# Performance work log

Measured on AMD Instinct MI355X. Metric: run time of the kernel, lower is better.

Reference implementation:

```python
import jax, jax.numpy as jnp
import numpy as np

B, T, N, M, P, YD = 256, 64, 128, 256, 256, 1


def lstm_cell(x, h, c, Wih, Whh, bih, bhh):
    # torch LSTM gate order: i, f, g, o
    gates = x @ Wih.T + h @ Whh.T + bih + bhh  # (B, 4H)
    i, f, g, o = jnp.split(gates, 4, axis=-1)
    c_new = jax.nn.sigmoid(f) * c + jax.nn.sigmoid(i) * jnp.tanh(g)
    h_new = jax.nn.sigmoid(o) * jnp.tanh(c_new)
    return h_new, c_new


def setup_inputs() -> dict:
    key = jax.random.key(0)
    ks = jax.random.split(key, 20)
    s = 0.05
    return {
        "inputs": jax.random.normal(ks[0], (B, T, N + YD), jnp.float32),
        "WU_e": jax.random.normal(ks[1], (T, 2 * M + T), jnp.float32) * s,
        "v_e": jax.random.normal(ks[2], (1, T), jnp.float32) * s,
        "Wih_e": jax.random.normal(ks[3], (4 * M, N), jnp.float32) * s,
        "Whh_e": jax.random.normal(ks[4], (4 * M, M), jnp.float32) * s,
        "bih_e": jax.random.normal(ks[5], (4 * M,), jnp.float32) * s,
        "bhh_e": jax.random.normal(ks[6], (4 * M,), jnp.float32) * s,
        "WU_d": jax.random.normal(ks[7], (M, 2 * P + M), jnp.float32) * s,
        "v_d": jax.random.normal(ks[8], (1, M), jnp.float32) * s,
        "wb_tilde": jax.random.normal(ks[9], (1, YD + M), jnp.float32) * s,
        "Wih_d": jax.random.normal(ks[10], (4 * P, 1), jnp.float32) * s,
        "Whh_d": jax.random.normal(ks[11], (4 * P, P), jnp.float32) * s,
        "bih_d": jax.random.normal(ks[12], (4 * P,), jnp.float32) * s,
        "bhh_d": jax.random.normal(ks[13], (4 * P,), jnp.float32) * s,
        "Wb_W": jax.random.normal(ks[14], (P, P + M), jnp.float32) * s,
        "Wb_b": jax.random.normal(ks[15], (P,), jnp.float32) * s,
        "vb_W": jax.random.normal(ks[16], (YD, P), jnp.float32) * s,
        "vb_b": jax.random.normal(ks[17], (YD,), jnp.float32) * s,
    }


def _darnn(inputs, WU_e, v_e, Wih_e, Whh_e, bih_e, bhh_e,
           WU_d, v_d, wb_tilde, Wih_d, Whh_d, bih_d, bhh_d,
           Wb_W, Wb_b, vb_W, vb_b):
    X = inputs[:, :, :N]          # (B, T, N)
    Y = inputs[:, :, N:]          # (B, T, YD)
    X_nt = jnp.transpose(X, (0, 2, 1))  # (B, N, T), constant across encoder steps

    # ---------------- Encoder ----------------
    def enc_step(carry, x_t):  # x_t: (B, N)
        h, c = carry
        hs = jnp.concatenate([h, c], axis=-1)  # (B, 2M)
        feat = jnp.concatenate(
            [jnp.broadcast_to(hs[:, None, :], (B, N, 2 * M)), X_nt], axis=-1)  # (B, N, 2M+T)
        E = (jnp.tanh(feat @ WU_e.T) @ v_e.T)[..., 0]  # (B, N)
        alpha = jax.nn.softmax(E, axis=1)
        h, c = lstm_cell(x_t * alpha, h, c, Wih_e, Whh_e, bih_e, bhh_e)
        return (h, c), h

    h0 = jnp.zeros((B, M), inputs.dtype)
    c0 = jnp.zeros((B, M), inputs.dtype)
    _, X_encoded = jax.lax.scan(enc_step, (h0, c0), jnp.transpose(X, (1, 0, 2)))
    Xe_bm = jnp.transpose(X_encoded, (1, 0, 2))  # (B, T, M)

    # ---------------- Decoder ----------------
    def dec_step(carry, y_t):  # y_t: (B, YD)
        h, c, _ = carry
        hs = jnp.concatenate([h, c], axis=-1)  # (B, 2P)
        feat = jnp.concatenate(
            [jnp.broadcast_to(hs[:, None, :], (B, T, 2 * P)), Xe_bm], axis=-1)  # (B, T, 2P+M)
        l = (jnp.tanh(feat @ WU_d.T) @ v_d.T)[..., 0]  # (B, T)
        beta = jax.nn.softmax(l, axis=1)
        ctx = jnp.einsum('bt,btm->bm', beta, Xe_bm)  # (B, M)
        y_tilde = jnp.concatenate([y_t, ctx], axis=-1) @ wb_tilde.T  # (B, 1)
        h, c = lstm_cell(y_tilde, h, c, Wih_d, Whh_d, bih_d, bhh_d)
        return (h, c, ctx), None

    hd0 = jnp.zeros((B, P), inputs.dtype)
    cd0 = jnp.zeros((B, P), inputs.dtype)
    ctx0 = jnp.zeros((B, M), inputs.dtype)
    (h, c, ctx), _ = jax.lax.scan(
        dec_step, (hd0, cd0, ctx0), jnp.transpose(Y[:, :T - 1, :], (1, 0, 2)))

    hidden = jnp.concatenate([h, ctx], axis=-1) @ Wb_W.T + Wb_b  # (B, P)
    y_hat = hidden @ vb_W.T + vb_b  # (B, YD)
    return y_hat


def reference(inputs, WU_e, v_e, Wih_e, Whh_e, bih_e, bhh_e,
              WU_d, v_d, wb_tilde, Wih_d, Whh_d, bih_d, bhh_d,
              Wb_W, Wb_b, vb_W, vb_b):
    return _darnn(inputs, WU_e, v_e, Wih_e, Whh_e, bih_e, bhh_e,
                  WU_d, v_d, wb_tilde, Wih_d, Whh_d, bih_d, bhh_d,
                  Wb_W, Wb_b, vb_W, vb_b)
```

## Files before the change

### kernel.cpp

```cpp
#include <hip/hip_runtime.h>
#include <math.h>


#define OFF_XWT   0u
#define OFF_XEWT  2097152u
#define OFF_XE    6291456u
#define OFF_HE    10485760u
#define OFF_HD    10616832u
#define OFF_SB    10747904u
#define OFF_SDB   10780672u
#define OFF_XA    10911744u
#define OFF_CTX   10944512u
#define OFF_YT    11010048u
#define OFF_BAR   11010304u
#define WS_END    11010816u

#define SENT_U 0x7FC00001u

#define SLAB_F 24576
#define PER_F  2432
#define SCR_F  12288
#define FLG_F  16
#define SMEM_F (SLAB_F + PER_F + SCR_F + FLG_F)
#define SMEM_BYTES (SMEM_F * 4)

#define F_E 0
#define F_L 1
#define F_B 2

__device__ __forceinline__ float fast_tanh(float x) {
  float xc = fminf(15.f, fmaxf(-15.f, x));
  float e = __expf(2.f * xc);
  return 1.f - 2.f * __builtin_amdgcn_rcpf(e + 1.f);
}
__device__ __forceinline__ float fast_sig(float x) {
  float xc = fminf(30.f, fmaxf(-30.f, x));
  return __builtin_amdgcn_rcpf(1.f + __expf(-xc));
}
__device__ __forceinline__ float wave_max(float v) {
#pragma unroll
  for (int o = 32; o; o >>= 1) v = fmaxf(v, __shfl_xor(v, o));
  return v;
}
__device__ __forceinline__ float wave_sum(float v) {
#pragma unroll
  for (int o = 32; o; o >>= 1) v += __shfl_xor(v, o);
  return v;
}
__device__ __forceinline__ float dot4(float4 a, float4 b) {
  return a.x*b.x + a.y*b.y + a.z*b.z + a.w*b.w;
}

__device__ __forceinline__ void st1_sc1(float* p, float v) {
  asm volatile("global_store_dword %0, %1, off sc1" :: "v"(p), "v"(v) : "memory");
}
__device__ __forceinline__ void ld1q_sc1(float4& a, const float* pa) {
  asm volatile("global_load_dwordx4 %0, %1, off sc1\n\ts_waitcnt vmcnt(0)"
               : "=&v"(a) : "v"(pa) : "memory");
}
__device__ __forceinline__ void ld1q_nw(float4& a, const float* pa) {
  asm volatile("global_load_dwordx4 %0, %1, off sc1"
               : "=&v"(a) : "v"(pa) : "memory");
}
__device__ __forceinline__ void vm0() {
  asm volatile("s_waitcnt vmcnt(0)" ::: "memory");
}
__device__ __forceinline__ void lgk0() {
  asm volatile("s_waitcnt lgkmcnt(0)" ::: "memory");
}
__device__ __forceinline__ float ld1s_sc1(const float* p) {
  float v;
  asm volatile("global_load_dword %0, %1, off sc1\n\ts_waitcnt vmcnt(0)"
               : "=&v"(v) : "v"(p) : "memory");
  return v;
}
__device__ __forceinline__ void ld8s_sc1(
    float& a0,float& a1,float& a2,float& a3,float& a4,float& a5,float& a6,float& a7,
    const float* p0,const float* p1,const float* p2,const float* p3,
    const float* p4,const float* p5,const float* p6,const float* p7) {
  asm volatile(
      "global_load_dword %0, %8, off sc1\n\t"
      "global_load_dword %1, %9, off sc1\n\t"
      "global_load_dword %2, %10, off sc1\n\t"
      "global_load_dword %3, %11, off sc1\n\t"
      "global_load_dword %4, %12, off sc1\n\t"
      "global_load_dword %5, %13, off sc1\n\t"
      "global_load_dword %6, %14, off sc1\n\t"
      "global_load_dword %7, %15, off sc1\n\t"
      "s_waitcnt vmcnt(0)"
      : "=&v"(a0),"=&v"(a1),"=&v"(a2),"=&v"(a3),
        "=&v"(a4),"=&v"(a5),"=&v"(a6),"=&v"(a7)
      : "v"(p0),"v"(p1),"v"(p2),"v"(p3),"v"(p4),"v"(p5),"v"(p6),"v"(p7)
      : "memory");
}
__device__ __forceinline__ void atomic_add_sc1(float* p, float v) {
  asm volatile("global_atomic_add_f32 %0, %1, off sc1" :: "v"(p), "v"(v) : "memory");
}

__device__ __forceinline__ void lds_inc(unsigned* f) {
  __hip_atomic_fetch_add(f, 1u, __ATOMIC_RELAXED, __HIP_MEMORY_SCOPE_WORKGROUP);
}
__device__ __forceinline__ void lds_poll(unsigned* f, unsigned tgt) {
  unsigned cur;
  do { cur = __hip_atomic_load(f, __ATOMIC_RELAXED, __HIP_MEMORY_SCOPE_WORKGROUP); } while (cur < tgt);
  asm volatile("" ::: "memory");
}

#define FMA16V(a0,a1,a2,a3,xv,wv) \
  a0.x += xv.x*wv.x; a0.y += xv.x*wv.y; a0.z += xv.x*wv.z; a0.w += xv.x*wv.w; \
  a1.x += xv.y*wv.x; a1.y += xv.y*wv.y; a1.z += xv.y*wv.z; a1.w += xv.y*wv.w; \
  a2.x += xv.z*wv.x; a2.y += xv.z*wv.y; a2.z += xv.z*wv.z; a2.w += xv.z*wv.w; \
  a3.x += xv.w*wv.x; a3.y += xv.w*wv.y; a3.z += xv.w*wv.z; a3.w += xv.w*wv.w;

__device__ __forceinline__ void bar_arrive(unsigned* bar) {
  asm volatile("s_waitcnt vmcnt(0)" ::: "memory");
  __syncthreads();
  if (threadIdx.x == 0)
    __hip_atomic_fetch_add(bar, 1u, __ATOMIC_RELAXED, __HIP_MEMORY_SCOPE_AGENT);
}
__device__ __forceinline__ void bar_wait(unsigned* bar, unsigned target) {
  if (threadIdx.x == 0) {
    unsigned cur;
    do {
      __builtin_amdgcn_s_sleep(1);
      cur = __hip_atomic_load(bar, __ATOMIC_RELAXED, __HIP_MEMORY_SCOPE_AGENT);
    } while (cur < target);
  }
  __syncthreads();
}

__global__ void darnn_init(float* __restrict__ ws, float* __restrict__ out) {
  unsigned i = blockIdx.x * 256u + threadIdx.x;
  const unsigned span = WS_END - OFF_HE;
  for (unsigned idx = i; idx < span; idx += gridDim.x * 256u) ws[OFF_HE + idx] = 0.f;
  if (i < 256u) out[i] = 0.f;
}

__global__ __launch_bounds__(512, 2) void darnn_main(
    const float* __restrict__ in,   const float* __restrict__ WUe,   const float* __restrict__ ve,
    const float* __restrict__ Wih_e,const float* __restrict__ Whh_e,
    const float* __restrict__ bih_e,const float* __restrict__ bhh_e,
    const float* __restrict__ WUd,  const float* __restrict__ vd,
    const float* __restrict__ wbt,  const float* __restrict__ Wih_d,
    const float* __restrict__ Whh_d,const float* __restrict__ bih_d, const float* __restrict__ bhh_d,
    const float* __restrict__ WbW,  const float* __restrict__ Wbb,
    const float* __restrict__ vbW,  const float* __restrict__ vbb,
    float* __restrict__ ws, float* __restrict__ out)
{
  extern __shared__ __align__(16) float sm[];
  float* SLAB = sm;
  float* PER  = sm + SLAB_F;
  float* SCR  = sm + SLAB_F + PER_F;
  unsigned* FLG = (unsigned*)(sm + SLAB_F + PER_F + SCR_F);
  const int tid = threadIdx.x;
  const int bid = blockIdx.x;
  const int grp = bid >> 4;
  const int mt  = bid & 15;
  const int b0  = grp << 4;
  const float SENTF = __uint_as_float(SENT_U);

  float* XWt  = ws + OFF_XWT;
  float* XeWt = ws + OFF_XEWT;
  float* Xe   = ws + OFF_XE;
  unsigned* barp = (unsigned*)(ws + OFF_BAR) + grp * 32;
  unsigned barn = 0;

  if (tid < FLG_F) FLG[tid] = 0u;

  float* wue_s  = PER;
  float* ve_s   = PER + 2304;
  float* bsum_e = PER + 2368;

  const int jfixE = ((tid & 63) + mt * 4) & 63;

  {
    int r = tid & 63, kq = tid >> 6;
    int grow = (r & 3) * 256 + mt * 16 + (r >> 2);
#pragma unroll 4
    for (int q = 0; q < 12; ++q) {
      int k = kq * 48 + q * 4;
      float4 wv = (k < 128) ? *(const float4*)(Wih_e + grow * 128 + k)
                            : *(const float4*)(Whh_e + grow * 256 + (k - 128));
      SLAB[(k + 0) * 64 + r] = wv.x; SLAB[(k + 1) * 64 + r] = wv.y;
      SLAB[(k + 2) * 64 + r] = wv.z; SLAB[(k + 3) * 64 + r] = wv.w;
    }
    {
      int lin = tid * 4;
      int j = lin >> 5, c0 = lin & 31;
      int col = (c0 < 16) ? (mt * 16 + c0) : (256 + mt * 16 + (c0 - 16));
      float4 wv = *(const float4*)(WUe + j * 576 + col);
      *(float4*)(wue_s + j * 36 + c0) = wv;
    }
    if (tid < 64) {
      ve_s[tid] = ve[tid];
      int g = tid >> 4, m2 = tid & 15, m = mt * 16 + m2;
      bsum_e[tid] = bih_e[g * 256 + m] + bhh_e[g * 256 + m];
    }
  }

  {
    float* Xs = SCR;
    const float* Xb = in + bid * 8256;
    __syncthreads();
    for (int it = 0; it < 16; ++it) {
      int lin = tid + it * 512;
      int k = lin >> 7, n = lin & 127;
      Xs[n * 68 + k] = Xb[k * 129 + n];
    }
    __syncthreads();
    int j = tid & 63, nh = tid >> 6;
    float acc[16];
#pragma unroll
    for (int i = 0; i < 16; ++i) acc[i] = 0.f;
    const float* wrow = WUe + j * 576 + 512;
    for (int kc = 0; kc < 4; ++kc) {
      float4 w0 = *(const float4*)(wrow + kc * 16 + 0);
      float4 w1 = *(const float4*)(wrow + kc * 16 + 4);
      float4 w2 = *(const float4*)(wrow + kc * 16 + 8);
      float4 w3 = *(const float4*)(wrow + kc * 16 + 12);
#pragma unroll
      for (int ni = 0; ni < 16; ++ni) {
        const float* xp = Xs + (nh * 16 + ni) * 68 + kc * 16;
        acc[ni] += dot4(*(const float4*)(xp + 0),  w0) + dot4(*(const float4*)(xp + 4),  w1)
                 + dot4(*(const float4*)(xp + 8),  w2) + dot4(*(const float4*)(xp + 12), w3);
      }
    }
    float* dst = XWt + bid * 8192 + j * 128 + nh * 16;
#pragma unroll
    for (int ni = 0; ni < 16; ++ni) dst[ni] = acc[ni];
    __syncthreads();
  }

  float4 whc[8];
#pragma unroll
  for (int q = 0; q < 8; ++q) whc[q] = *(const float4*)(wue_s + jfixE * 36 + q * 4);
  float4 bsE = {0,0,0,0};
  {
    int m2 = tid & 15;
    bsE.x = bsum_e[m2]; bsE.y = bsum_e[16 + m2];
    bsE.z = bsum_e[32 + m2]; bsE.w = bsum_e[48 + m2];
  }
  float xwreg[32];
  if (tid < 256) {
    int w = tid >> 6, l = tid & 63;
    const float* xwp = XWt + bid * 8192;
#pragma unroll
    for (int jj = 0; jj < 16; ++jj) {
      xwreg[jj]      = xwp[(w * 16 + jj) * 128 + l];
      xwreg[16 + jj] = xwp[(w * 16 + jj) * 128 + 64 + l];
    }
  }
  float c_reg = 0.f;

  for (int t = 0; t < 64; ++t) {
    const int rd = t & 1, wr2 = (t + 1) & 1;
    float* xah = SCR + 1024;
    const int ks = tid >> 6, ml = (tid >> 2) & 15, b4 = tid & 3;
    float4 a0 = {0,0,0,0}, a1 = {0,0,0,0}, a2 = {0,0,0,0}, a3 = {0,0,0,0};

    bar_wait(barp, barn);

    if (tid < 256) {
      int w = tid >> 6, l = tid & 63;
      float* Sj = SCR;
      float* Ep = SCR + 64;
      if (l < 16)
        Sj[w * 16 + l] = ld1s_sc1(ws + OFF_SB + (unsigned)rd * 16384 + (unsigned)bid * 64 + w * 16 + l);
      lgk0();
      float e0 = 0.f, e1 = 0.f;
#pragma unroll
      for (int jj = 0; jj < 16; ++jj) {
        float s = Sj[w * 16 + jj];
        float vv = ve_s[w * 16 + jj];
        e0 += vv * fast_tanh(xwreg[jj] + s);
        e1 += vv * fast_tanh(xwreg[16 + jj] + s);
      }
      Ep[w * 128 + l] = e0;
      Ep[w * 128 + 64 + l] = e1;
      lgk0();
      if (l == 0) lds_inc(FLG + F_E);
      if (w == 0) {
        lds_poll(FLG + F_E, 4u * (t + 1));
        float En0 = Ep[l] + Ep[128 + l] + Ep[256 + l] + Ep[384 + l];
        float En1 = Ep[64 + l] + Ep[192 + l] + Ep[320 + l] + Ep[448 + l];
        float mx = wave_max(fmaxf(En0, En1));
        float ex0 = __expf(En0 - mx), ex1 = __expf(En1 - mx);
        float tot = wave_sum(ex0 + ex1);
        float rt = __builtin_amdgcn_rcpf(tot);
        float x0 = in[bid * 8256 + t * 129 + l];
        float x1 = in[bid * 8256 + t * 129 + 64 + l];
        float* XAg = ws + OFF_XA + (unsigned)grp * 2048;
        st1_sc1(XAg + l * 16 + mt, x0 * ex0 * rt);
        st1_sc1(XAg + (64 + l) * 16 + mt, x1 * ex1 * rt);
        vm0();
        if (tid == 0)
          __hip_atomic_fetch_add(barp, 1u, __ATOMIC_RELAXED, __HIP_MEMORY_SCOPE_AGENT);
      }
    } else {
      int u = tid - 256;
      float4 h0, h1, h2, h3;
      const float* hb = ws + OFF_HE + (unsigned)rd * 65536 + (unsigned)grp * 4096 + u * 16;
      ld1q_nw(h0, hb); ld1q_nw(h1, hb + 4); ld1q_nw(h2, hb + 8); ld1q_nw(h3, hb + 12);
      vm0();
      float* row = xah + (unsigned)(128 + u) * 20;
      *(float4*)(row + 0) = h0; *(float4*)(row + 4) = h1;
      *(float4*)(row + 8) = h2; *(float4*)(row + 12) = h3;
      lgk0();
      int s = u >> 6;
      const float* xp = xah + (unsigned)(128 + s * 64) * 20 + b4 * 4;
      const float* wp = SLAB + (unsigned)(128 + s * 64) * 64 + ml * 4;
#pragma unroll 8
      for (int kk = 0; kk < 64; ++kk) {
        float4 xv = *(const float4*)(xp + kk * 20);
        float4 wv = *(const float4*)(wp + kk * 64);
        FMA16V(a0, a1, a2, a3, xv, wv);
      }
    }
    barn += 16;
    bar_wait(barp, barn);

    if (tid < 16) {
      float* sp = ws + OFF_SB + (unsigned)rd * 16384 + (unsigned)bid * 64 + tid * 4;
      float z01 = (t == 63 && tid == 0) ? SENTF : 0.f;
      st1_sc1(sp + 0, z01); st1_sc1(sp + 1, z01);
      st1_sc1(sp + 2, 0.f); st1_sc1(sp + 3, 0.f);
    }
    {
      int l = tid & 63;
      int k = (ks << 4) + (l >> 2), i4 = (l & 3) * 4;
      float4 q;
      ld1q_sc1(q, ws + OFF_XA + (unsigned)grp * 2048 + k * 16 + i4);
      *(float4*)(xah + k * 20 + i4) = q;
      lgk0();
    }
    {
      const float* xp = xah + (unsigned)(ks * 16) * 20 + b4 * 4;
      const float* wp = SLAB + (unsigned)(ks * 16) * 64 + ml * 4;
#pragma unroll 8
      for (int kk = 0; kk < 16; ++kk) {
        float4 xv = *(const float4*)(xp + kk * 20);
        float4 wv = *(const float4*)(wp + kk * 64);
        FMA16V(a0, a1, a2, a3, xv, wv);
      }
    }
    __syncthreads();
    float* red = SCR;
    {
      float* rp = red + (unsigned)(ks * 64 + ml * 4 + b4) * 20;
      *(float4*)(rp + 0) = a0; *(float4*)(rp + 4) = a1;
      *(float4*)(rp + 8) = a2; *(float4*)(rp + 12) = a3;
    }
    __syncthreads();
    float* hcs = SCR + 10240;
    if (tid < 256) {
      int m2 = tid & 15, bl = tid >> 4;
      int t2 = m2 * 4 + (bl >> 2), bs = bl & 3;
      float4 gate = {0,0,0,0};
#pragma unroll
      for (int k2 = 0; k2 < 8; ++k2) {
        float4 rr = *(const float4*)(red + (unsigned)(k2 * 64 + t2) * 20 + bs * 4);
        gate.x += rr.x; gate.y += rr.y; gate.z += rr.z; gate.w += rr.w;
      }
      float gi = gate.x + bsE.x, gf = gate.y + bsE.y;
      float gg = gate.z + bsE.z, go = gate.w + bsE.w;
      float cn = fast_sig(gf) * c_reg + fast_sig(gi) * fast_tanh(gg);
      float hn = fast_sig(go) * fast_tanh(cn);
      c_reg = cn;
      unsigned m = mt * 16 + m2;
      st1_sc1(ws + OFF_HE + (unsigned)wr2 * 65536 + (unsigned)grp * 4096 + m * 16 + bl, hn);
      st1_sc1(Xe + ((unsigned)(b0 + bl) * 64 + t) * 256 + m, hn);
      hcs[bl * 32 + m2] = hn;
      hcs[bl * 32 + 16 + m2] = cn;
    }
    __syncthreads();
    {
      int wq = tid >> 6;
#pragma unroll
      for (int e2 = 0; e2 < 2; ++e2) {
        int bl2 = wq * 2 + e2;
        const float* hp = hcs + bl2 * 32;
        float s = 0.f;
#pragma unroll
        for (int q = 0; q < 4; ++q) {
          s += dot4(*(const float4*)(hp + q * 4), whc[q]);
          s += dot4(*(const float4*)(hp + 16 + q * 4), whc[4 + q]);
        }
        atomic_add_sc1(ws + OFF_SB + (unsigned)wr2 * 16384 + (unsigned)(b0 + bl2) * 64 + jfixE, s);
      }
    }
    barn += 16;
    bar_arrive(barp);
  }
  bar_wait(barp, barn);

  float xe[64];
  if (tid < 256) {
    const float* xb = Xe + (unsigned)bid * 16384 + tid;
#pragma unroll
    for (int g8 = 0; g8 < 8; ++g8) {
      ld8s_sc1(xe[g8*8+0], xe[g8*8+1], xe[g8*8+2], xe[g8*8+3],
               xe[g8*8+4], xe[g8*8+5], xe[g8*8+6], xe[g8*8+7],
               xb + (g8*8+0)*256, xb + (g8*8+1)*256, xb + (g8*8+2)*256,
               xb + (g8*8+3)*256, xb + (g8*8+4)*256, xb + (g8*8+5)*256,
               xb + (g8*8+6)*256, xb + (g8*8+7)*256);
    }
  }

  float* vd_s   = PER;
  float* wbt_s  = PER + 256;
  float* bsum_d = PER + 520;
  float* wihd_s = PER + 584;
  float* q_s    = PER + 704;
  float* qpart  = PER + 768;
  float* wudT   = SLAB + 16384;
  const int jfixD = ((tid & 255) + mt * 16) & 255;
  __syncthreads();
  {
    int r = tid & 63, kq = tid >> 6;
    int grow = (r & 3) * 256 + mt * 16 + (r >> 2);
#pragma unroll 4
    for (int q = 0; q < 8; ++q) {
      int k = kq * 32 + q * 4;
      float4 wv = *(const float4*)(Whh_d + grow * 256 + k);
      SLAB[(k + 0) * 64 + r] = wv.x; SLAB[(k + 1) * 64 + r] = wv.y;
      SLAB[(k + 2) * 64 + r] = wv.z; SLAB[(k + 3) * 64 + r] = wv.w;
    }
    {
      int j = tid & 255, half = tid >> 8;
#pragma unroll
      for (int i = 0; i < 16; ++i) {
        int c = half * 16 + i;
        int col = (c < 16) ? (mt * 16 + c) : (256 + mt * 16 + (c - 16));
        wudT[c * 256 + j] = WUd[(unsigned)j * 768 + col];
      }
    }
    if (tid < 256) vd_s[tid] = vd[tid];
    if (tid < 257) wbt_s[tid] = wbt[tid];
    if (tid < 64) {
      int g = tid >> 4, m2 = tid & 15, m = mt * 16 + m2;
      bsum_d[tid] = bih_d[g * 256 + m] + bhh_d[g * 256 + m];
      wihd_s[tid] = Wih_d[g * 256 + m];
    }
  }
  __syncthreads();

  if (tid < 256) {
    int w = tid >> 6, l = tid & 63;
    float wm = wbt_s[1 + tid];
#pragma unroll
    for (int t4 = 0; t4 < 64; ++t4) {
      float v = wave_sum(wm * xe[t4]);
      if (l == 0) qpart[w * 64 + t4] = v;
    }
  }
  __syncthreads();
  if (tid < 64) q_s[tid] = qpart[tid] + qpart[64 + tid] + qpart[128 + tid] + qpart[192 + tid];
  __syncthreads();

  {
    float* XeT = SCR;
    float* Wdc = SCR + 4096;
    int tt2 = tid & 15, jq = tid >> 4;
    for (int jc = 0; jc < 2; ++jc) {
      float4 c0 = {0,0,0,0}, c1 = {0,0,0,0}, c2 = {0,0,0,0}, c3 = {0,0,0,0};
      for (int kc = 0; kc < 4; ++kc) {
        __syncthreads();
        if (tid < 256 && (tid >> 6) == kc) {
          int kk = tid & 63;
#pragma unroll
          for (int t4 = 0; t4 < 16; ++t4) {
            float4 v = { xe[t4*4+0], xe[t4*4+1], xe[t4*4+2], xe[t4*4+3] };
            *(float4*)(XeT + kk * 64 + t4 * 4) = v;
          }
        }
        {
          int jj = tid >> 2, k16 = (tid & 3) * 16;
          const float* src = WUd + (unsigned)(jc * 128 + jj) * 768 + 512 + kc * 64 + k16;
#pragma unroll
          for (int s4 = 0; s4 < 4; ++s4) {
            float4 wv = *(const float4*)(src + s4 * 4);
            Wdc[(k16 + s4*4 + 0) * 128 + jj] = wv.x;
            Wdc[(k16 + s4*4 + 1) * 128 + jj] = wv.y;
            Wdc[(k16 + s4*4 + 2) * 128 + jj] = wv.z;
            Wdc[(k16 + s4*4 + 3) * 128 + jj] = wv.w;
          }
        }
        __syncthreads();
#pragma unroll 8
        for (int kk = 0; kk < 64; ++kk) {
          float4 xv = *(const float4*)(XeT + kk * 64 + tt2 * 4);
          float4 wv = *(const float4*)(Wdc + kk * 128 + jq * 4);
          FMA16V(c0, c1, c2, c3, wv, xv);
        }
      }
      int jb = jc * 128 + jq * 4;
      *(float4*)(XeWt + ((unsigned)bid * 256 + jb + 0) * 64 + tt2 * 4) = c0;
      *(float4*)(XeWt + ((unsigned)bid * 256 + jb + 1) * 64 + tt2 * 4) = c1;
      *(float4*)(XeWt + ((unsigned)bid * 256 + jb + 2) * 64 + tt2 * 4) = c2;
      *(float4*)(XeWt + ((unsigned)bid * 256 + jb + 3) * 64 + tt2 * 4) = c3;
    }
    __syncthreads();
  }

  float wreg[32];
#pragma unroll
  for (int c = 0; c < 32; ++c) wreg[c] = wudT[c * 256 + jfixD];
  float4 bsD = {0,0,0,0}, wiD = {0,0,0,0};
  {
    int m2 = tid & 15;
    bsD.x = bsum_d[m2]; bsD.y = bsum_d[16 + m2]; bsD.z = bsum_d[32 + m2]; bsD.w = bsum_d[48 + m2];
    wiD.x = wihd_s[m2]; wiD.y = wihd_s[16 + m2]; wiD.z = wihd_s[32 + m2]; wiD.w = wihd_s[48 + m2];
  }
  float xewreg[64];
  if (tid < 256) {
    int w = tid >> 6, l = tid & 63;
    const float* xew = XeWt + (unsigned)bid * 16384 + l;
#pragma unroll
    for (int jj = 0; jj < 64; ++jj) xewreg[jj] = xew[(w * 64 + jj) << 6];
  }
  float q_reg = 0.f, yv = 0.f;
  if (tid < 64) {
    q_reg = q_s[tid];
    if (tid < 63) yv = in[bid * 8256 + tid * 129 + 128];
  }
  const float wbt0 = wbt_s[0];
  float cd_reg = 0.f;

  for (int t = 0; t < 63; ++t) {
    const int rd = t & 1, wr2 = (t + 1) & 1;
    const int ml = (tid >> 2) & 15, b4 = tid & 3;
    float* hT  = SCR + 2048;
    float* red = SCR + 7168;

    bar_wait(barp, barn);

    if (tid < 256) {
      int w = tid >> 6, l = tid & 63;
      float* Sdj  = SCR;
      float* lp   = SCR + 256;
      float* beta = SCR + 512;
      Sdj[w * 64 + l] = ld1s_sc1(ws + OFF_SDB + (unsigned)rd * 65536 + (unsigned)bid * 256 + w * 64 + l);
      lgk0();
      float lpar = 0.f;
#pragma unroll 8
      for (int jj = 0; jj < 64; ++jj)
        lpar += vd_s[w * 64 + jj] * fast_tanh(xewreg[jj] + Sdj[w * 64 + jj]);
      lp[w * 64 + l] = lpar;
      lgk0();
      if (l == 0) lds_inc(FLG + F_L);
      if (w == 0) {
        lds_poll(FLG + F_L, 4u * (t + 1));
        float lv = lp[l] + lp[64 + l] + lp[128 + l] + lp[192 + l];
        float mx = wave_max(lv);
        float ex = __expf(lv - mx);
        float sw = wave_sum(ex);
        float rt = __builtin_amdgcn_rcpf(sw);
        float ytn = wave_sum(ex * q_reg);
        if (l == 0) {
          float yt = wbt0 * __shfl(yv, t) + ytn * rt;
          st1_sc1(ws + OFF_SB + 16384u + (unsigned)bid * 64u + (unsigned)rd, yt);
        }
        if (t == 62) {
          beta[l] = ex * rt;
          lgk0();
          if (l == 0) lds_inc(FLG + F_B);
        }
      }
      if (t == 62) {
        lds_poll(FLG + F_B, 1u);
        lgk0();
        float ctx = 0.f;
#pragma unroll
        for (int tt = 0; tt < 64; ++tt) ctx += beta[tt] * xe[tt];
        st1_sc1(ws + OFF_CTX + (unsigned)bid * 256 + tid, ctx);
      }
    } else {
      if (tid == 256)
        st1_sc1(ws + OFF_SB + 16384u + (unsigned)bid * 64u + (unsigned)wr2, SENTF);
      int u = tid - 256;
      float4 h0, h1, h2, h3;
      const float* hb = ws + OFF_HD + (unsigned)rd * 65536 + (unsigned)grp * 4096 + u * 16;
      ld1q_nw(h0, hb); ld1q_nw(h1, hb + 4); ld1q_nw(h2, hb + 8); ld1q_nw(h3, hb + 12);
      vm0();
      float* row = hT + (unsigned)u * 20;
      *(float4*)(row + 0) = h0; *(float4*)(row + 4) = h1;
      *(float4*)(row + 8) = h2; *(float4*)(row + 12) = h3;
      lgk0();
      int s = u >> 6;
      float4 a0 = {0,0,0,0}, a1 = {0,0,0,0}, a2 = {0,0,0,0}, a3 = {0,0,0,0};
      const float* xp = hT + (unsigned)(s * 64) * 20 + b4 * 4;
      const float* wp = SLAB + (unsigned)(s * 64) * 64 + ml * 4;
#pragma unroll 8
      for (int kk = 0; kk < 64; ++kk) {
        float4 xv = *(const float4*)(xp + kk * 20);
        float4 wv = *(const float4*)(wp + kk * 64);
        FMA16V(a0, a1, a2, a3, xv, wv);
      }
      float* rp = red + (unsigned)(s * 64 + ml * 4 + b4) * 20;
      *(float4*)(rp + 0) = a0; *(float4*)(rp + 4) = a1;
      *(float4*)(rp + 8) = a2; *(float4*)(rp + 12) = a3;
    }
    if (tid < 64) {
      float* sp = ws + OFF_SDB + (unsigned)rd * 65536 + (unsigned)bid * 256 + tid * 4;
      st1_sc1(sp + 0, 0.f); st1_sc1(sp + 1, 0.f);
      st1_sc1(sp + 2, 0.f); st1_sc1(sp + 3, 0.f);
    }
    __syncthreads();

    float* hcs = SCR;
    if (tid < 256) {
      int m2 = tid & 15, bl = tid >> 4;
      int t2 = m2 * 4 + (bl >> 2), bs = bl & 3;
      float4 gate = {0,0,0,0};
#pragma unroll
      for (int k2 = 0; k2 < 4; ++k2) {
        float4 rr = *(const float4*)(red + (unsigned)(k2 * 64 + t2) * 20 + bs * 4);
        gate.x += rr.x; gate.y += rr.y; gate.z += rr.z; gate.w += rr.w;
      }
      const float* pyt = ws + OFF_SB + 16384u + (unsigned)(b0 + bl) * 64u + (unsigned)rd;
      float yt_reg = ld1s_sc1(pyt);
      while (__float_as_uint(yt_reg) == SENT_U) {
        __builtin_amdgcn_s_sleep(4);
        yt_reg = ld1s_sc1(pyt);
      }
      float gi = gate.x + yt_reg * wiD.x + bsD.x;
      float gf = gate.y + yt_reg * wiD.y + bsD.y;
      float gg = gate.z + yt_reg * wiD.z + bsD.z;
      float go = gate.w + yt_reg * wiD.w + bsD.w;
      float cn = fast_sig(gf) * cd_reg + fast_sig(gi) * fast_tanh(gg);
      float hn = fast_sig(go) * fast_tanh(cn);
      cd_reg = cn;
      unsigned m = mt * 16 + m2;
      st1_sc1(ws + OFF_HD + (unsigned)wr2 * 65536 + (unsigned)grp * 4096 + m * 16 + bl, hn);
      hcs[bl * 32 + m2] = hn;
      hcs[bl * 32 + 16 + m2] = cn;
    }
    __syncthreads();
    {
      int half = tid >> 8;
#pragma unroll
      for (int e2 = 0; e2 < 8; ++e2) {
        int bl2 = half * 8 + e2;
        const float* hp = hcs + bl2 * 32;
        float s = 0.f;
#pragma unroll
        for (int c = 0; c < 16; ++c) s += hp[c] * wreg[c];
#pragma unroll
        for (int c = 0; c < 16; ++c) s += hp[16 + c] * wreg[16 + c];
        atomic_add_sc1(ws + OFF_SDB + (unsigned)wr2 * 65536 + (unsigned)(b0 + bl2) * 256 + jfixD, s);
      }
    }
    barn += 16;
    bar_arrive(barp);
  }
  bar_wait(barp, barn);

  {
    float* hsf  = SCR;
    float* hid2 = SCR + 8256;
    {
      int l0 = tid * 2, l1 = tid * 2 + 1;
      int k0 = l0 >> 2, i0 = l0 & 3, k1 = l1 >> 2, i1 = l1 & 3;
      const float* hb = ws + OFF_HD + 65536u + (unsigned)grp * 4096;
      int bl0 = l0 >> 6, c0 = (l0 & 63) * 4, bl1 = l1 >> 6, c1 = (l1 & 63) * 4;
      float4 qa, qb, qc, qd;
      ld1q_nw(qa, hb + k0 * 16 + i0 * 4);
      ld1q_nw(qb, hb + k1 * 16 + i1 * 4);
      ld1q_nw(qc, ws + OFF_CTX + (unsigned)(b0 + bl0) * 256 + c0);
      ld1q_nw(qd, ws + OFF_CTX + (unsigned)(b0 + bl1) * 256 + c1);
      vm0();
      hsf[(i0 * 4 + 0) * 516 + k0] = qa.x; hsf[(i0 * 4 + 1) * 516 + k0] = qa.y;
      hsf[(i0 * 4 + 2) * 516 + k0] = qa.z; hsf[(i0 * 4 + 3) * 516 + k0] = qa.w;
      hsf[(i1 * 4 + 0) * 516 + k1] = qb.x; hsf[(i1 * 4 + 1) * 516 + k1] = qb.y;
      hsf[(i1 * 4 + 2) * 516 + k1] = qb.z; hsf[(i1 * 4 + 3) * 516 + k1] = qb.w;
      *(float4*)(hsf + bl0 * 516 + 256 + c0) = qc;
      *(float4*)(hsf + bl1 * 516 + 256 + c1) = qd;
    }
    __syncthreads();
    int bl = tid & 15, p4 = (tid >> 4) & 15, half = tid >> 8;
    int row = mt * 16 + p4;
    const float* wrow = WbW + (unsigned)row * 512 + half * 256;
    const float* hp = hsf + bl * 516 + half * 256;
    float acc = half ? 0.f : Wbb[row];
#pragma unroll 8
    for (int q = 0; q < 64; ++q)
      acc += dot4(*(const float4*)(hp + q * 4), *(const float4*)(wrow + q * 4));
    hid2[half * 272 + bl * 17 + p4] = acc;
    __syncthreads();
    if (tid < 16) {
      float s = 0.f;
#pragma unroll
      for (int p = 0; p < 16; ++p)
        s += (hid2[tid * 17 + p] + hid2[272 + tid * 17 + p]) * vbW[mt * 16 + p];
      if (mt == 0) s += vbb[0];
      atomicAdd(&out[b0 + tid], s);
    }
  }
}

extern "C" void kernel_launch(void* const* d_in, const int* in_sizes, int n_in,
                              void* d_out, int out_size, void* d_ws, size_t ws_size,
                              hipStream_t stream) {
  (void)in_sizes; (void)n_in; (void)out_size; (void)ws_size;
  const float* in    = (const float*)d_in[0];
  const float* WUe   = (const float*)d_in[1];
  const float* ve    = (const float*)d_in[2];
  const float* Wih_e = (const float*)d_in[3];
  const float* Whh_e = (const float*)d_in[4];
  const float* bih_e = (const float*)d_in[5];
  const float* bhh_e = (const float*)d_in[6];
  const float* WUd   = (const float*)d_in[7];
  const float* vd    = (const float*)d_in[8];
  const float* wbt   = (const float*)d_in[9];
  const float* Wih_d = (const float*)d_in[10];
  const float* Whh_d = (const float*)d_in[11];
  const float* bih_d = (const float*)d_in[12];
  const float* bhh_d = (const float*)d_in[13];
  const float* WbW   = (const float*)d_in[14];
  const float* Wbb   = (const float*)d_in[15];
  const float* vbW   = (const float*)d_in[16];
  const float* vbb   = (const float*)d_in[17];
  float* ws  = (float*)d_ws;
  float* out = (float*)d_out;

  (void)hipFuncSetAttribute((const void*)darnn_main,
                            hipFuncAttributeMaxDynamicSharedMemorySize, SMEM_BYTES);
  hipLaunchKernelGGL(darnn_init, dim3(1024), dim3(256), 0, stream, ws, out);
  hipLaunchKernelGGL(darnn_main, dim3(256), dim3(512), SMEM_BYTES, stream,
                     in, WUe, ve, Wih_e, Whh_e, bih_e, bhh_e,
                     WUd, vd, wbt, Wih_d, Whh_d, bih_d, bhh_d,
                     WbW, Wbb, vbW, vbb, ws, out);
}
```

Measured before the change: 1.241 ms.

## Replace global atomic-add reductions with per-tile partial stores summed by readers

The encoder and decoder attention score accumulations previously used global float atomics into a shared buffer, followed by explicit zeroing every step. Each of the 16 tiles now writes its partial sum to a dedicated slot, reusing the XWt/XeWt workspace regions, and the consumer loads and reduces the 16 partials itself, using vector loads plus wave shuffles in the encoder. This removes atomic contention and the per-step re-zeroing stores. In exchange it adds more global read traffic per step, an extra initial zero pass in init, and a barrier arrive before the decoder loop. It also relies on those workspace regions being dead by the time they are reused.

Measured after the change: 2.030 ms. 63.6% more time.

```diff
diff --git a/kernel.cpp b/kernel.cpp
--- a/kernel.cpp
+++ b/kernel.cpp
@@ -93,9 +93,6 @@
       : "v"(p0),"v"(p1),"v"(p2),"v"(p3),"v"(p4),"v"(p5),"v"(p6),"v"(p7)
       : "memory");
 }
-__device__ __forceinline__ void atomic_add_sc1(float* p, float v) {
-  asm volatile("global_atomic_add_f32 %0, %1, off sc1" :: "v"(p), "v"(v) : "memory");
-}
 
 __device__ __forceinline__ void lds_inc(unsigned* f) {
   __hip_atomic_fetch_add(f, 1u, __ATOMIC_RELAXED, __HIP_MEMORY_SCOPE_WORKGROUP);
@@ -133,6 +130,10 @@
   unsigned i = blockIdx.x * 256u + threadIdx.x;
   const unsigned span = WS_END - OFF_HE;
   for (unsigned idx = i; idx < span; idx += gridDim.x * 256u) ws[OFF_HE + idx] = 0.f;
+  for (unsigned idx = i; idx < 262144u; idx += gridDim.x * 256u) {
+    unsigned g = idx >> 14, off = idx & 16383u;
+    ws[OFF_XEWT + g * 262144u + off] = 0.f;
+  }
   if (i < 256u) out[i] = 0.f;
 }
 
@@ -162,6 +163,8 @@
   float* XWt  = ws + OFF_XWT;
   float* XeWt = ws + OFF_XEWT;
   float* Xe   = ws + OFF_XE;
+  float* EP = ws + OFF_XEWT + (unsigned)grp * 262144u;
+  float* DP = ws + OFF_XWT  + (unsigned)grp * 131072u;
   unsigned* barp = (unsigned*)(ws + OFF_BAR) + grp * 32;
   unsigned barn = 0;
 
@@ -264,9 +267,17 @@
       int w = tid >> 6, l = tid & 63;
       float* Sj = SCR;
       float* Ep = SCR + 64;
-      if (l < 16)
-        Sj[w * 16 + l] = ld1s_sc1(ws + OFF_SB + (unsigned)rd * 16384 + (unsigned)bid * 64 + w * 16 + l);
-      lgk0();
+      {
+        int jj0 = l & 15, q = l >> 4;
+        float4 pq;
+        ld1q_sc1(pq, EP + (unsigned)rd * 16384u + (unsigned)mt * 1024u
+                        + (unsigned)(w * 16 + jj0) * 16u + (unsigned)(q * 4));
+        float ps = pq.x + pq.y + pq.z + pq.w;
+        ps += __shfl_xor(ps, 16);
+        ps += __shfl_xor(ps, 32);
+        if (l < 16) Sj[w * 16 + l] = ps;
+        lgk0();
+      }
       float e0 = 0.f, e1 = 0.f;
 #pragma unroll
       for (int jj = 0; jj < 16; ++jj) {
@@ -319,11 +330,9 @@
     barn += 16;
     bar_wait(barp, barn);
 
-    if (tid < 16) {
-      float* sp = ws + OFF_SB + (unsigned)rd * 16384 + (unsigned)bid * 64 + tid * 4;
-      float z01 = (t == 63 && tid == 0) ? SENTF : 0.f;
-      st1_sc1(sp + 0, z01); st1_sc1(sp + 1, z01);
-      st1_sc1(sp + 2, 0.f); st1_sc1(sp + 3, 0.f);
+    if (t == 63 && tid == 0) {
+      float* sp = ws + OFF_SB + 16384u + (unsigned)bid * 64u;
+      st1_sc1(sp + 0, SENTF); st1_sc1(sp + 1, SENTF);
     }
     {
       int l = tid & 63;
@@ -385,7 +394,8 @@
           s += dot4(*(const float4*)(hp + q * 4), whc[q]);
           s += dot4(*(const float4*)(hp + 16 + q * 4), whc[4 + q]);
         }
-        atomic_add_sc1(ws + OFF_SB + (unsigned)wr2 * 16384 + (unsigned)(b0 + bl2) * 64 + jfixE, s);
+        st1_sc1(EP + (unsigned)wr2 * 16384u + (unsigned)bl2 * 1024u
+                   + (unsigned)jfixE * 16u + (unsigned)mt, s);
       }
     }
     barn += 16;
@@ -526,6 +536,14 @@
   const float wbt0 = wbt_s[0];
   float cd_reg = 0.f;
 
+  {
+    float* dp0 = DP + (unsigned)mt * 4096u;
+#pragma unroll
+    for (int i8 = 0; i8 < 8; ++i8) st1_sc1(dp0 + (unsigned)(i8 * 512 + tid), 0.f);
+    barn += 16;
+    bar_arrive(barp);
+  }
+
   for (int t = 0; t < 63; ++t) {
     const int rd = t & 1, wr2 = (t + 1) & 1;
     const int ml = (tid >> 2) & 15, b4 = tid & 3;
@@ -539,8 +557,16 @@
       float* Sdj  = SCR;
       float* lp   = SCR + 256;
       float* beta = SCR + 512;
-      Sdj[w * 64 + l] = ld1s_sc1(ws + OFF_SDB + (unsigned)rd * 65536 + (unsigned)bid * 256 + w * 64 + l);
-      lgk0();
+      {
+        int j = w * 64 + l;
+        const float* dpb = DP + (unsigned)rd * 65536u + (unsigned)mt * 4096u + (unsigned)j * 16u;
+        float4 p0, p1, p2, p3;
+        ld1q_nw(p0, dpb); ld1q_nw(p1, dpb + 4); ld1q_nw(p2, dpb + 8); ld1q_nw(p3, dpb + 12);
+        vm0();
+        Sdj[j] = (p0.x + p0.y + p0.z + p0.w) + (p1.x + p1.y + p1.z + p1.w)
+               + (p2.x + p2.y + p2.z + p2.w) + (p3.x + p3.y + p3.z + p3.w);
+        lgk0();
+      }
       float lpar = 0.f;
 #pragma unroll 8
       for (int jj = 0; jj < 64; ++jj)
@@ -600,11 +626,6 @@
       *(float4*)(rp + 0) = a0; *(float4*)(rp + 4) = a1;
       *(float4*)(rp + 8) = a2; *(float4*)(rp + 12) = a3;
     }
-    if (tid < 64) {
-      float* sp = ws + OFF_SDB + (unsigned)rd * 65536 + (unsigned)bid * 256 + tid * 4;
-      st1_sc1(sp + 0, 0.f); st1_sc1(sp + 1, 0.f);
-      st1_sc1(sp + 2, 0.f); st1_sc1(sp + 3, 0.f);
-    }
     __syncthreads();
 
     float* hcs = SCR;
@@ -647,7 +668,8 @@
         for (int c = 0; c < 16; ++c) s += hp[c] * wreg[c];
 #pragma unroll
         for (int c = 0; c < 16; ++c) s += hp[16 + c] * wreg[16 + c];
-        atomic_add_sc1(ws + OFF_SDB + (unsigned)wr2 * 65536 + (unsigned)(b0 + bl2) * 256 + jfixD, s);
+        st1_sc1(DP + (unsigned)wr2 * 65536u + (unsigned)bl2 * 4096u
+                   + (unsigned)jfixD * 16u + (unsigned)mt, s);
       }
     }
     barn += 16;
```
